# Performance work log

Measured on AMD Instinct MI355X. Metric: run time of the kernel, lower is better.

The kernel has to match this reference:

```python
import jax, jax.numpy as jnp
import numpy as np

N = 16384
NODE_DIM = 128
OUT_DIM = 128
NUM_HEADS = 8
HEAD_DIM = OUT_DIM // NUM_HEADS  # 16
NUM_CLASSES = 40
LN_EPS = 1e-6


def _layer_norm(x, scale, eps=LN_EPS):
    # flax LayerNorm with use_bias=False, use_scale=True
    mean = jnp.mean(x, axis=-1, keepdims=True)
    var = jnp.mean(jnp.square(x - mean), axis=-1, keepdims=True)
    return (x - mean) * jax.lax.rsqrt(var + eps) * scale


def setup_inputs() -> dict:
    key = jax.random.key(0)
    ks = jax.random.split(key, 10)
    s = 0.02
    return {
        "x": jax.random.normal(ks[0], (N, NODE_DIM), jnp.float32),
        "adj": jax.random.uniform(ks[1], (N, N), jnp.float32),
        "Wq": jax.random.normal(ks[2], (NODE_DIM, OUT_DIM), jnp.float32) * s,
        "Wk": jax.random.normal(ks[3], (NODE_DIM, OUT_DIM), jnp.float32) * s,
        "Wv": jax.random.normal(ks[4], (NODE_DIM, OUT_DIM), jnp.float32) * s,
        "Wo": jax.random.normal(ks[5], (OUT_DIM, NODE_DIM), jnp.float32) * s,
        "ln1_scale": jnp.ones((NODE_DIM,), jnp.float32),
        "W1": jax.random.normal(ks[6], (NODE_DIM, NODE_DIM * 2), jnp.float32) * s,
        "W2": jax.random.normal(ks[7], (NODE_DIM * 2, NODE_DIM), jnp.float32) * s,
        "ln2_scale": jnp.ones((NODE_DIM,), jnp.float32),
        "Wout": jax.random.normal(ks[8], (NODE_DIM, NUM_CLASSES), jnp.float32) * s,
    }


def reference(x, adj, Wq, Wk, Wv, Wo, ln1_scale, W1, W2, ln2_scale, Wout):
    # Graph aggregation: adj @ x  -> [N, node_dim]
    h0 = adj @ x

    # MHA: elementwise q*k "attention", softmax over heads axis
    q = (h0 @ Wq).reshape(-1, HEAD_DIM, NUM_HEADS)
    k = (h0 @ Wk).reshape(-1, HEAD_DIM, NUM_HEADS)
    v = (h0 @ Wv).reshape(-1, HEAD_DIM, NUM_HEADS)
    scores = q * k / jnp.sqrt(jnp.float32(HEAD_DIM))
    w = jax.nn.softmax(scores, axis=-1)  # softmax over heads (last axis)
    attn = (w * v).reshape(-1, OUT_DIM)

    h = attn @ Wo
    h = _layer_norm(h + h0, ln1_scale)

    # FFN
    h1 = h
    h = jax.nn.relu(h @ W1) @ W2
    h = _layer_norm(h + h1, ln2_scale)

    return h @ Wout
```

## Files before the change

kernel.cpp:

```cpp
#include <hip/hip_runtime.h>


typedef __bf16 bf16x8 __attribute__((ext_vector_type(8)));
typedef float  f32x16 __attribute__((ext_vector_type(16)));
typedef float  f32x4  __attribute__((ext_vector_type(4)));

#define GN 16384
#define GD 128
#define BM 128
#define BK 32
#define KSPLIT 8
#define KRANGE (GN / KSPLIT)
#define NSUP (KRANGE / 64)

__device__ __forceinline__ unsigned short f2bf(float f) {
    unsigned u = __float_as_uint(f);
    unsigned r = (u + 0x7FFFu + ((u >> 16) & 1u)) >> 16;
    return (unsigned short)r;
}
__device__ __forceinline__ float bf2f(unsigned short u) {
    return __uint_as_float(((unsigned)u) << 16);
}

typedef __attribute__((address_space(1))) const void glb_cv;
typedef __attribute__((address_space(3))) void lds_v;
__device__ __forceinline__ void gload_lds16(const void* g, void* l) {
    __builtin_amdgcn_global_load_lds((glb_cv*)g, (lds_v*)l, 16, 0, 0);
}

__global__ void prep_x(const float* __restrict__ x,
                       unsigned short* __restrict__ xh,
                       unsigned short* __restrict__ xl) {
    const int kt = blockIdx.x;
    const int c  = threadIdx.x;
    float v[32];
#pragma unroll
    for (int i = 0; i < 32; ++i)
        v[i] = x[((long)kt * 32 + i) * 128 + c];
    const int f = (c >> 1) & 3;
    unsigned short* oh = xh + (long)kt * 4096 + c * 32;
    unsigned short* ol = xl + (long)kt * 4096 + c * 32;
#pragma unroll
    for (int g = 0; g < 4; ++g) {
        uint4 ph, pl;
        unsigned hp[4], lp[4];
#pragma unroll
        for (int q = 0; q < 4; ++q) {
            float a = v[g * 8 + q * 2], b = v[g * 8 + q * 2 + 1];
            unsigned short ha = f2bf(a), hb = f2bf(b);
            float la = a - bf2f(ha), lb = b - bf2f(hb);
            hp[q] = (unsigned)ha | ((unsigned)hb << 16);
            lp[q] = (unsigned)f2bf(la) | ((unsigned)f2bf(lb) << 16);
        }
        ph.x = hp[0]; ph.y = hp[1]; ph.z = hp[2]; ph.w = hp[3];
        pl.x = lp[0]; pl.y = lp[1]; pl.z = lp[2]; pl.w = lp[3];
        const int gp = g ^ f;
        *(uint4*)&oh[gp * 8] = ph;
        *(uint4*)&ol[gp * 8] = pl;
    }
}

__global__ __launch_bounds__(256, 2) void gemm_adj(
    const float* __restrict__ adj,
    const unsigned short* __restrict__ xh,
    const unsigned short* __restrict__ xl,
    float* __restrict__ cpart) {
    __shared__ __align__(16) float Afp[BM * 64];
    __shared__ __align__(16) unsigned short Bh[2][GD * BK];
    __shared__ __align__(16) unsigned short Bl[2][GD * BK];

    const int t   = threadIdx.x;
    const int b   = blockIdx.x;
    const int ks  = b & 7;
    const int bmi = b >> 3;
    const long rowbase = (long)bmi * BM;
    const int kb0 = ks * KRANGE;
    const int lane = t & 63, wid = t >> 6;
    const int rm  = wid * 32 + (lane & 31);
    const int hl  = lane >> 5;
    const int l16 = lane & 15;
    const int rloc = lane >> 4;

    f32x16 acc[4];
#pragma unroll
    for (int n = 0; n < 4; ++n)
#pragma unroll
        for (int e = 0; e < 16; ++e) acc[n][e] = 0.0f;

    for (int sup = 0; sup < NSUP; ++sup) {
        const int kb = kb0 + sup * 64;
#pragma unroll
        for (int j = 0; j < 8; ++j) {
            const int rr  = wid * 32 + j * 4 + rloc;
            const int gch = l16 ^ (rr & 7);
            const float* src = adj + (rowbase + rr) * 16384L + kb + gch * 4;
            gload_lds16(src, ((char*)Afp) + wid * 8192 + j * 1024);
        }
#pragma unroll
        for (int half = 0; half < 2; ++half) {
            const long tile = (long)(kb0 >> 5) + sup * 2 + half;
            const char* sh = (const char*)(xh + tile * 4096);
            const char* sl = (const char*)(xl + tile * 4096);
#pragma unroll
            for (int j = 0; j < 2; ++j) {
                const int seg = wid + j * 4;
                gload_lds16(sh + seg * 1024 + lane * 16,
                            ((char*)&Bh[half][0]) + seg * 1024);
                gload_lds16(sl + seg * 1024 + lane * 16,
                            ((char*)&Bl[half][0]) + seg * 1024);
            }
        }
        __syncthreads();
#pragma unroll
        for (int half = 0; half < 2; ++half) {
#pragma unroll
            for (int s = 0; s < 2; ++s) {
                const int c16 = half * 8 + s * 4 + hl * 2;
                const int ca = (c16     ) ^ (rm & 7);
                const int cb = (c16 + 1) ^ (rm & 7);
                const f32x4 a0 = *(const f32x4*)((const char*)Afp + rm * 256 + ca * 16);
                const f32x4 a1 = *(const f32x4*)((const char*)Afp + rm * 256 + cb * 16);
                bf16x8 am, al;
#pragma unroll
                for (int jj = 0; jj < 4; ++jj) {
                    const __bf16 h0 = (__bf16)a0[jj];
                    am[jj] = h0;
                    al[jj] = (__bf16)(a0[jj] - (float)h0);
                    const __bf16 h1 = (__bf16)a1[jj];
                    am[4 + jj] = h1;
                    al[4 + jj] = (__bf16)(a1[jj] - (float)h1);
                }
                const int hh = s * 2 + hl;
#pragma unroll
                for (int n = 0; n < 4; ++n) {
                    const int c = n * 32 + (lane & 31);
                    const int bidx = c * 32 + (hh ^ ((c >> 1) & 3)) * 8;
                    const bf16x8 bn  = *(const bf16x8*)&Bh[half][bidx];
                    const bf16x8 bl4 = *(const bf16x8*)&Bl[half][bidx];
                    acc[n] = __builtin_amdgcn_mfma_f32_32x32x16_bf16(am, bn,  acc[n], 0, 0, 0);
                    acc[n] = __builtin_amdgcn_mfma_f32_32x32x16_bf16(am, bl4, acc[n], 0, 0, 0);
                    acc[n] = __builtin_amdgcn_mfma_f32_32x32x16_bf16(al, bn,  acc[n], 0, 0, 0);
                }
            }
        }
        __syncthreads();
    }
    float* cp = cpart + (long)ks * GN * GD;
#pragma unroll
    for (int n = 0; n < 4; ++n) {
        const int c = n * 32 + (lane & 31);
#pragma unroll
        for (int e = 0; e < 16; ++e) {
            const int rl = wid * 32 + (e & 3) + 8 * (e >> 2) + 4 * (lane >> 5);
            __builtin_nontemporal_store(acc[n][e], &cp[(rowbase + rl) * (long)GD + c]);
        }
    }
}

__global__ __launch_bounds__(256, 2) void tail_fused(
    const float* __restrict__ cpart,
    const float* __restrict__ Wq, const float* __restrict__ Wk,
    const float* __restrict__ Wv, const float* __restrict__ Wo,
    const float* __restrict__ ln1s,
    const float* __restrict__ W1, const float* __restrict__ W2,
    const float* __restrict__ ln2s, const float* __restrict__ Wout,
    float* __restrict__ out) {
    __shared__ __align__(16) float H[32][128];
    __shared__ __align__(16) float C[32][128];
    __shared__ __align__(16) float FB[32 * 256];
    float (*B1)[128] = (float (*)[128])FB;

    const int t = threadIdx.x;
    const int ogrp = t & 31, rowgrp = t >> 5;
    const int o4 = ogrp * 4, rbase = rowgrp * 4;
    const long r0 = (long)blockIdx.x * 32;

#pragma unroll
    for (int j = 0; j < 4; ++j) {
        const int p = t + 256 * j;
        const int row = p >> 5, c4 = (p & 31) * 4;
        f32x4 s = __builtin_nontemporal_load(
            (const f32x4*)&cpart[(r0 + row) * 128 + c4]);
#pragma unroll
        for (int ks = 1; ks < KSPLIT; ++ks) {
            f32x4 v = __builtin_nontemporal_load(
                (const f32x4*)&cpart[((long)ks * GN + r0 + row) * 128 + c4]);
            s += v;
        }
        *(f32x4*)&H[row][c4] = s;
    }
    __syncthreads();

    float qa[4][4] = {}, ka[4][4] = {};
    for (int dg = 0; dg < 32; ++dg) {
        f32x4 h4[4];
#pragma unroll
        for (int rr = 0; rr < 4; ++rr) h4[rr] = *(const f32x4*)&H[rbase + rr][dg * 4];
#pragma unroll
        for (int i = 0; i < 4; ++i) {
            const int d = dg * 4 + i;
            const f32x4 wq = *(const f32x4*)&Wq[d * 128 + o4];
            const f32x4 wk = *(const f32x4*)&Wk[d * 128 + o4];
#pragma unroll
            for (int rr = 0; rr < 4; ++rr) {
                const float hv = h4[rr][i];
                qa[rr][0] += hv * wq[0]; qa[rr][1] += hv * wq[1];
                qa[rr][2] += hv * wq[2]; qa[rr][3] += hv * wq[3];
                ka[rr][0] += hv * wk[0]; ka[rr][1] += hv * wk[1];
                ka[rr][2] += hv * wk[2]; ka[rr][3] += hv * wk[3];
            }
        }
    }
    float w[4][4];
#pragma unroll
    for (int rr = 0; rr < 4; ++rr) {
        float s0 = qa[rr][0] * ka[rr][0] * 0.25f;
        float s1 = qa[rr][1] * ka[rr][1] * 0.25f;
        float s2 = qa[rr][2] * ka[rr][2] * 0.25f;
        float s3 = qa[rr][3] * ka[rr][3] * 0.25f;
        float m = fmaxf(fmaxf(s0, s1), fmaxf(s2, s3));
        m = fmaxf(m, __shfl_xor(m, 1, 64));
        float e0 = __expf(s0 - m), e1 = __expf(s1 - m);
        float e2 = __expf(s2 - m), e3 = __expf(s3 - m);
        float sum = e0 + e1 + e2 + e3;
        sum += __shfl_xor(sum, 1, 64);
        float inv = 1.0f / sum;
        w[rr][0] = e0 * inv; w[rr][1] = e1 * inv;
        w[rr][2] = e2 * inv; w[rr][3] = e3 * inv;
    }
    {
        float va[4][4] = {};
        for (int dg = 0; dg < 32; ++dg) {
            f32x4 h4[4];
#pragma unroll
            for (int rr = 0; rr < 4; ++rr) h4[rr] = *(const f32x4*)&H[rbase + rr][dg * 4];
#pragma unroll
            for (int i = 0; i < 4; ++i) {
                const int d = dg * 4 + i;
                const f32x4 wv = *(const f32x4*)&Wv[d * 128 + o4];
#pragma unroll
                for (int rr = 0; rr < 4; ++rr) {
                    const float hv = h4[rr][i];
                    va[rr][0] += hv * wv[0]; va[rr][1] += hv * wv[1];
                    va[rr][2] += hv * wv[2]; va[rr][3] += hv * wv[3];
                }
            }
        }
#pragma unroll
        for (int rr = 0; rr < 4; ++rr) {
            f32x4 a;
            a[0] = w[rr][0] * va[rr][0]; a[1] = w[rr][1] * va[rr][1];
            a[2] = w[rr][2] * va[rr][2]; a[3] = w[rr][3] * va[rr][3];
            *(f32x4*)&B1[rbase + rr][o4] = a;
        }
    }
    __syncthreads();
    {
        float oa[4][4] = {};
        for (int dg = 0; dg < 32; ++dg) {
            f32x4 h4[4];
#pragma unroll
            for (int rr = 0; rr < 4; ++rr) h4[rr] = *(const f32x4*)&B1[rbase + rr][dg * 4];
#pragma unroll
            for (int i = 0; i < 4; ++i) {
                const int d = dg * 4 + i;
                const f32x4 wo = *(const f32x4*)&Wo[d * 128 + o4];
#pragma unroll
                for (int rr = 0; rr < 4; ++rr) {
                    const float hv = h4[rr][i];
                    oa[rr][0] += hv * wo[0]; oa[rr][1] += hv * wo[1];
                    oa[rr][2] += hv * wo[2]; oa[rr][3] += hv * wo[3];
                }
            }
        }
        const f32x4 g1 = *(const f32x4*)&ln1s[o4];
#pragma unroll
        for (int rr = 0; rr < 4; ++rr) {
            const f32x4 hres = *(const f32x4*)&H[rbase + rr][o4];
            float u0 = oa[rr][0] + hres[0], u1 = oa[rr][1] + hres[1];
            float u2 = oa[rr][2] + hres[2], u3 = oa[rr][3] + hres[3];
            float s1 = u0 + u1 + u2 + u3;
            float s2 = u0 * u0 + u1 * u1 + u2 * u2 + u3 * u3;
#pragma unroll
            for (int mk = 1; mk < 32; mk <<= 1) {
                s1 += __shfl_xor(s1, mk, 64);
                s2 += __shfl_xor(s2, mk, 64);
            }
            const float mean = s1 * (1.f / 128.f);
            const float var  = s2 * (1.f / 128.f) - mean * mean;
            const float rstd = rsqrtf(var + 1e-6f);
            f32x4 cvr;
            cvr[0] = (u0 - mean) * rstd * g1[0]; cvr[1] = (u1 - mean) * rstd * g1[1];
            cvr[2] = (u2 - mean) * rstd * g1[2]; cvr[3] = (u3 - mean) * rstd * g1[3];
            *(f32x4*)&C[rbase + rr][o4] = cvr;
        }
    }
    __syncthreads();
#pragma unroll
    for (int h = 0; h < 2; ++h) {
        float fa[4][4] = {};
        for (int dg = 0; dg < 32; ++dg) {
            f32x4 h4[4];
#pragma unroll
            for (int rr = 0; rr < 4; ++rr) h4[rr] = *(const f32x4*)&C[rbase + rr][dg * 4];
#pragma unroll
            for (int i = 0; i < 4; ++i) {
                const int d = dg * 4 + i;
                const f32x4 w1 = *(const f32x4*)&W1[d * 256 + h * 128 + o4];
#pragma unroll
                for (int rr = 0; rr < 4; ++rr) {
                    const float hv = h4[rr][i];
                    fa[rr][0] += hv * w1[0]; fa[rr][1] += hv * w1[1];
                    fa[rr][2] += hv * w1[2]; fa[rr][3] += hv * w1[3];
                }
            }
        }
#pragma unroll
        for (int rr = 0; rr < 4; ++rr) {
            f32x4 a;
            a[0] = fmaxf(fa[rr][0], 0.f); a[1] = fmaxf(fa[rr][1], 0.f);
            a[2] = fmaxf(fa[rr][2], 0.f); a[3] = fmaxf(fa[rr][3], 0.f);
            *(f32x4*)&FB[(rbase + rr) * 256 + h * 128 + o4] = a;
        }
        __syncthreads();
    }
    {
        float ga[4][4] = {};
        for (int dg = 0; dg < 64; ++dg) {
            f32x4 f4[4];
#pragma unroll
            for (int rr = 0; rr < 4; ++rr)
                f4[rr] = *(const f32x4*)&FB[(rbase + rr) * 256 + dg * 4];
#pragma unroll
            for (int i = 0; i < 4; ++i) {
                const int d = dg * 4 + i;
                const f32x4 w2 = *(const f32x4*)&W2[d * 128 + o4];
#pragma unroll
                for (int rr = 0; rr < 4; ++rr) {
                    const float hv = f4[rr][i];
                    ga[rr][0] += hv * w2[0]; ga[rr][1] += hv * w2[1];
                    ga[rr][2] += hv * w2[2]; ga[rr][3] += hv * w2[3];
                }
            }
        }
        const f32x4 g2 = *(const f32x4*)&ln2s[o4];
#pragma unroll
        for (int rr = 0; rr < 4; ++rr) {
            const f32x4 cres = *(const f32x4*)&C[rbase + rr][o4];
            float u0 = ga[rr][0] + cres[0], u1 = ga[rr][1] + cres[1];
            float u2 = ga[rr][2] + cres[2], u3 = ga[rr][3] + cres[3];
            float s1 = u0 + u1 + u2 + u3;
            float s2 = u0 * u0 + u1 * u1 + u2 * u2 + u3 * u3;
#pragma unroll
            for (int mk = 1; mk < 32; mk <<= 1) {
                s1 += __shfl_xor(s1, mk, 64);
                s2 += __shfl_xor(s2, mk, 64);
            }
            const float mean = s1 * (1.f / 128.f);
            const float var  = s2 * (1.f / 128.f) - mean * mean;
            const float rstd = rsqrtf(var + 1e-6f);
            f32x4 cvr;
            cvr[0] = (u0 - mean) * rstd * g2[0]; cvr[1] = (u1 - mean) * rstd * g2[1];
            cvr[2] = (u2 - mean) * rstd * g2[2]; cvr[3] = (u3 - mean) * rstd * g2[3];
            *(f32x4*)&C[rbase + rr][o4] = cvr;
        }
    }
    __syncthreads();
    {
        const int r7 = t >> 3, ob = t & 7;
        float acc[5] = {0.f, 0.f, 0.f, 0.f, 0.f};
        for (int dg = 0; dg < 32; ++dg) {
            const f32x4 c4 = *(const f32x4*)&C[r7][dg * 4];
#pragma unroll
            for (int i = 0; i < 4; ++i) {
                const int d = dg * 4 + i;
                const float hv = c4[i];
#pragma unroll
                for (int jj = 0; jj < 5; ++jj)
                    acc[jj] += hv * Wout[d * 40 + ob + 8 * jj];
            }
        }
#pragma unroll
        for (int jj = 0; jj < 5; ++jj)
            out[(r0 + r7) * 40 + ob + 8 * jj] = acc[jj];
    }
}

extern "C" void kernel_launch(void* const* d_in, const int* in_sizes, int n_in,
                              void* d_out, int out_size, void* d_ws, size_t ws_size,
                              hipStream_t stream) {
    const float* x    = (const float*)d_in[0];
    const float* adj  = (const float*)d_in[1];
    const float* Wq   = (const float*)d_in[2];
    const float* Wk   = (const float*)d_in[3];
    const float* Wv   = (const float*)d_in[4];
    const float* Wo   = (const float*)d_in[5];
    const float* ln1s = (const float*)d_in[6];
    const float* W1   = (const float*)d_in[7];
    const float* W2   = (const float*)d_in[8];
    const float* ln2s = (const float*)d_in[9];
    const float* Wout = (const float*)d_in[10];

    char* ws = (char*)d_ws;
    unsigned short* xh = (unsigned short*)(ws);
    unsigned short* xl = (unsigned short*)(ws + (4L << 20));
    float* cpart       = (float*)(ws + (8L << 20));

    prep_x<<<512, 128, 0, stream>>>(x, xh, xl);
    gemm_adj<<<1024, 256, 0, stream>>>(adj, xh, xl, cpart);
    tail_fused<<<512, 256, 0, stream>>>(cpart, Wq, Wk, Wv, Wo, ln1s,
                                        W1, W2, ln2s, Wout, (float*)d_out);
}
```

Baseline: 387.4 us.

## Double-buffer adj GEMM loads and halve split-K with single-block occupancy

Adds double-buffered LDS stages to the adjacency GEMM so the next 64-wide K chunk is prefetched asynchronously while MFMAs run on the current one, using explicit vmcnt waits and raw barriers. Split-K drops from 8 to 4 and the grid is halved, with launch bounds relaxed to one block per SIMD, because the doubled LDS footprint limits occupancy. Partial-sum stores and loads switch from nontemporal to normal accesses. The aim is to hide global-load latency and reduce partial-sum traffic in the reduction, at the cost of fewer resident waves and fewer blocks to spread across CUs.

```diff
diff --git a/kernel.cpp b/kernel.cpp
--- a/kernel.cpp
+++ b/kernel.cpp
@@ -9,7 +9,7 @@
 #define GD 128
 #define BM 128
 #define BK 32
-#define KSPLIT 8
+#define KSPLIT 4
 #define KRANGE (GN / KSPLIT)
 #define NSUP (KRANGE / 64)
 
@@ -60,19 +60,19 @@
     }
 }
 
-__global__ __launch_bounds__(256, 2) void gemm_adj(
+__global__ __launch_bounds__(256, 1) void gemm_adj(
     const float* __restrict__ adj,
     const unsigned short* __restrict__ xh,
     const unsigned short* __restrict__ xl,
     float* __restrict__ cpart) {
-    __shared__ __align__(16) float Afp[BM * 64];
-    __shared__ __align__(16) unsigned short Bh[2][GD * BK];
-    __shared__ __align__(16) unsigned short Bl[2][GD * BK];
+    __shared__ __align__(16) float Afp[2][BM * 64];
+    __shared__ __align__(16) unsigned short Bh[2][2][GD * BK];
+    __shared__ __align__(16) unsigned short Bl[2][2][GD * BK];
 
     const int t   = threadIdx.x;
     const int b   = blockIdx.x;
-    const int ks  = b & 7;
-    const int bmi = b >> 3;
+    const int ks  = b & 3;
+    const int bmi = b >> 2;
     const long rowbase = (long)bmi * BM;
     const int kb0 = ks * KRANGE;
     const int lane = t & 63, wid = t >> 6;
@@ -87,14 +87,14 @@
 #pragma unroll
         for (int e = 0; e < 16; ++e) acc[n][e] = 0.0f;
 
-    for (int sup = 0; sup < NSUP; ++sup) {
+    auto STAGE = [&](int sup, int buf) {
         const int kb = kb0 + sup * 64;
 #pragma unroll
         for (int j = 0; j < 8; ++j) {
             const int rr  = wid * 32 + j * 4 + rloc;
             const int gch = l16 ^ (rr & 7);
             const float* src = adj + (rowbase + rr) * 16384L + kb + gch * 4;
-            gload_lds16(src, ((char*)Afp) + wid * 8192 + j * 1024);
+            gload_lds16(src, ((char*)&Afp[buf][0]) + wid * 8192 + j * 1024);
         }
 #pragma unroll
         for (int half = 0; half < 2; ++half) {
@@ -105,12 +105,29 @@
             for (int j = 0; j < 2; ++j) {
                 const int seg = wid + j * 4;
                 gload_lds16(sh + seg * 1024 + lane * 16,
-                            ((char*)&Bh[half][0]) + seg * 1024);
+                            ((char*)&Bh[buf][half][0]) + seg * 1024);
                 gload_lds16(sl + seg * 1024 + lane * 16,
-                            ((char*)&Bl[half][0]) + seg * 1024);
-            }
-        }
-        __syncthreads();
+                            ((char*)&Bl[buf][half][0]) + seg * 1024);
+            }
+        }
+    };
+
+    STAGE(0, 0);
+    for (int sup = 0; sup < NSUP; ++sup) {
+        const int p = sup & 1;
+        __builtin_amdgcn_sched_barrier(0);
+        __builtin_amdgcn_s_barrier();
+        __builtin_amdgcn_sched_barrier(0);
+        if (sup + 1 < NSUP) {
+            STAGE(sup + 1, p ^ 1);
+            __builtin_amdgcn_sched_barrier(0);
+            asm volatile("s_waitcnt vmcnt(16)" ::: "memory");
+        } else {
+            asm volatile("s_waitcnt vmcnt(0)" ::: "memory");
+        }
+        __builtin_amdgcn_sched_barrier(0);
+        __builtin_amdgcn_s_barrier();
+        __builtin_amdgcn_sched_barrier(0);
 #pragma unroll
         for (int half = 0; half < 2; ++half) {
 #pragma unroll
@@ -118,8 +135,8 @@
                 const int c16 = half * 8 + s * 4 + hl * 2;
                 const int ca = (c16     ) ^ (rm & 7);
                 const int cb = (c16 + 1) ^ (rm & 7);
-                const f32x4 a0 = *(const f32x4*)((const char*)Afp + rm * 256 + ca * 16);
-                const f32x4 a1 = *(const f32x4*)((const char*)Afp + rm * 256 + cb * 16);
+                const f32x4 a0 = *(const f32x4*)((const char*)&Afp[p][0] + rm * 256 + ca * 16);
+                const f32x4 a1 = *(const f32x4*)((const char*)&Afp[p][0] + rm * 256 + cb * 16);
                 bf16x8 am, al;
 #pragma unroll
                 for (int jj = 0; jj < 4; ++jj) {
@@ -135,15 +152,14 @@
                 for (int n = 0; n < 4; ++n) {
                     const int c = n * 32 + (lane & 31);
                     const int bidx = c * 32 + (hh ^ ((c >> 1) & 3)) * 8;
-                    const bf16x8 bn  = *(const bf16x8*)&Bh[half][bidx];
-                    const bf16x8 bl4 = *(const bf16x8*)&Bl[half][bidx];
+                    const bf16x8 bn  = *(const bf16x8*)&Bh[p][half][bidx];
+                    const bf16x8 bl4 = *(const bf16x8*)&Bl[p][half][bidx];
                     acc[n] = __builtin_amdgcn_mfma_f32_32x32x16_bf16(am, bn,  acc[n], 0, 0, 0);
                     acc[n] = __builtin_amdgcn_mfma_f32_32x32x16_bf16(am, bl4, acc[n], 0, 0, 0);
                     acc[n] = __builtin_amdgcn_mfma_f32_32x32x16_bf16(al, bn,  acc[n], 0, 0, 0);
                 }
             }
         }
-        __syncthreads();
     }
     float* cp = cpart + (long)ks * GN * GD;
 #pragma unroll
@@ -152,7 +168,7 @@
 #pragma unroll
         for (int e = 0; e < 16; ++e) {
             const int rl = wid * 32 + (e & 3) + 8 * (e >> 2) + 4 * (lane >> 5);
-            __builtin_nontemporal_store(acc[n][e], &cp[(rowbase + rl) * (long)GD + c]);
+            cp[(rowbase + rl) * (long)GD + c] = acc[n][e];
         }
     }
 }
@@ -179,14 +195,10 @@
     for (int j = 0; j < 4; ++j) {
         const int p = t + 256 * j;
         const int row = p >> 5, c4 = (p & 31) * 4;
-        f32x4 s = __builtin_nontemporal_load(
-            (const f32x4*)&cpart[(r0 + row) * 128 + c4]);
-#pragma unroll
-        for (int ks = 1; ks < KSPLIT; ++ks) {
-            f32x4 v = __builtin_nontemporal_load(
-                (const f32x4*)&cpart[((long)ks * GN + r0 + row) * 128 + c4]);
-            s += v;
-        }
+        f32x4 s = *(const f32x4*)&cpart[(r0 + row) * 128 + c4];
+#pragma unroll
+        for (int ks = 1; ks < KSPLIT; ++ks)
+            s += *(const f32x4*)&cpart[((long)ks * GN + r0 + row) * 128 + c4];
         *(f32x4*)&H[row][c4] = s;
     }
     __syncthreads();
@@ -407,7 +419,7 @@
     float* cpart       = (float*)(ws + (8L << 20));
 
     prep_x<<<512, 128, 0, stream>>>(x, xh, xl);
-    gemm_adj<<<1024, 256, 0, stream>>>(adj, xh, xl, cpart);
+    gemm_adj<<<512, 256, 0, stream>>>(adj, xh, xl, cpart);
     tail_fused<<<512, 256, 0, stream>>>(cpart, Wq, Wk, Wv, Wo, ln1s,
                                         W1, W2, ln2s, Wout, (float*)d_out);
 }
```

Measured after the change: 540.1 us. +39.4%, slower.
